# Kernel tuning notes

Hardware: AMD Instinct MI355X
Metric: run time of the kernel (lower is better)

Reference implementation:

```python
import jax, jax.numpy as jnp
import numpy as np

NUM_CLASSES = 5
SMOOTH = 1e-5


def setup_inputs() -> dict:
    key = jax.random.key(0)
    k1, k2, k3 = jax.random.split(key, 3)
    B, C, X, Y, Z = 2, NUM_CLASSES, 128, 128, 128
    net_output = jax.random.normal(k1, (B, C, X, Y, Z), dtype=jnp.float32)
    target = jax.random.randint(k2, (B, 1, X, Y, Z), 0, C, dtype=jnp.int64)
    dist = jax.random.uniform(k3, (B, 1, X, Y, Z), dtype=jnp.float32)
    return {"net_output": net_output, "target": target, "dist": dist}


def reference(net_output, target, dist):
    # --- Distance-map penalized multi-class Dice ---
    p = jax.nn.softmax(net_output, axis=1)  # (B,C,X,Y,Z)
    gt = target[:, 0]  # (B,X,Y,Z)
    classes = jnp.arange(NUM_CLASSES)[None, :, None, None, None]
    y_onehot = (gt[:, None] == classes).astype(p.dtype)  # (B,C,X,Y,Z)
    # per-class, per-batch sums over spatial dims
    tp = jnp.sum(p * y_onehot * dist, axis=(2, 3, 4))  # (B,C), dist broadcasts over C
    denom = jnp.sum(p, axis=(2, 3, 4)) + jnp.sum(y_onehot, axis=(2, 3, 4))  # (B,C)
    dc = (2.0 * tp + SMOOTH) / (denom + SMOOTH)  # (B,C)
    # sum over classes of batch-mean, divided by num_classes == overall mean
    dpdc_loss = -jnp.mean(dc)
    # --- Cross entropy (mean over all voxels), target squeezed to class idx ---
    logp = jax.nn.log_softmax(net_output, axis=1)  # (B,C,X,Y,Z)
    nll = -jnp.take_along_axis(logp, target, axis=1)  # (B,1,X,Y,Z)
    ce_loss = jnp.mean(nll)
    # aggregate == 'sum', weight_ce = weight_dice = 1
    return ce_loss + dpdc_loss
```

## Files before the change

kernel.cpp:

```cpp
#include <hip/hip_runtime.h>

#define NC 5
#define NB 2
#define SPATIAL (128*128*128)
#define TILE_VOX 512
#define NTILES (SPATIAL/TILE_VOX)
#define SMOOTHF 1e-5f

#define TILE_BYTES (16*1024)


__device__ __forceinline__ void async16(const char* g, char* l) {
    __builtin_amdgcn_global_load_lds(
        (const __attribute__((address_space(1))) void*)g,
        (__attribute__((address_space(3))) void*)l, 16, 0, 0);
}

__global__ __launch_bounds__(256) void dpdc_main(
    const float* __restrict__ net, const void* __restrict__ targ,
    const float* __restrict__ dist, float* __restrict__ slots, int TPB)
{
    __shared__ __align__(16) char lds[2][TILE_BYTES];
    const int b = blockIdx.y, tid = threadIdx.x;

    const unsigned long long tv = ((const unsigned long long*)targ)[tid & 63];
    const int t64 = (__ballot(tv >= 5ull) == 0ull);

    const char* netb  = (const char*)net  + (size_t)b * NC * SPATIAL * 4;
    const char* distb = (const char*)dist + (size_t)b * SPATIAL * 4;
    const char* targb = (const char*)targ + (size_t)b * SPATIAL * (t64 ? 8 : 4);

    const int tl0 = blockIdx.x * TPB;
    const int nchunk = t64 ? 1024 : 896;

    const char* srcp[4];
    int sstr[4];
    bool act[4];
    #pragma unroll
    for (int k = 0; k < 4; ++k) {
        const int q = tid + 256 * k;
        act[k] = (q < nchunk);
        const int r = q >> 7;
        if (r < 5) {
            srcp[k] = netb + (size_t)r * SPATIAL * 4
                           + (size_t)tl0 * 2048 + (size_t)(q & 127) * 16;
            sstr[k] = 2048;
        } else if (r == 5) {
            srcp[k] = distb + (size_t)tl0 * 2048 + (size_t)(q & 127) * 16;
            sstr[k] = 2048;
        } else {
            const int tstr = t64 ? 4096 : 2048;
            srcp[k] = targb + (size_t)tl0 * tstr + (size_t)(q - 768) * 16;
            sstr[k] = tstr;
        }
    }

    auto stage = [&](int bf) {
        char* base = &lds[bf][0];
        #pragma unroll
        for (int k = 0; k < 4; ++k)
            if (act[k]) async16(srcp[k], base + (size_t)(tid + 256 * k) * 16);
        #pragma unroll
        for (int k = 0; k < 4; ++k) srcp[k] += sstr[k];
    };

    float tp[NC], sp[NC], cnt[NC];
    #pragma unroll
    for (int c = 0; c < NC; ++c) { tp[c] = 0.f; sp[c] = 0.f; cnt[c] = 0.f; }
    float nll = 0.f;

    stage(0);
    __syncthreads();

    #pragma unroll 1
    for (int k = 0; k < TPB; ++k) {
        if (k + 1 < TPB) stage((k + 1) & 1);

        const char* base = &lds[k & 1][0];
        float2 l[NC];
        #pragma unroll
        for (int c = 0; c < NC; ++c)
            l[c] = *(const float2*)(base + c * 2048 + tid * 8);
        float2 dd = *(const float2*)(base + 10240 + tid * 8);
        int tt[2];
        if (t64) {
            ulonglong2 a = *(const ulonglong2*)(base + 12288 + tid * 16);
            tt[0] = (int)a.x; tt[1] = (int)a.y;
        } else {
            int2 a = *(const int2*)(base + 12288 + tid * 8);
            tt[0] = a.x; tt[1] = a.y;
        }
        const float* dv = (const float*)&dd;
        #pragma unroll
        for (int j = 0; j < 2; ++j) {
            float lc[NC];
            #pragma unroll
            for (int c = 0; c < NC; ++c) lc[c] = ((const float*)&l[c])[j];
            float m = fmaxf(fmaxf(fmaxf(lc[0], lc[1]), fmaxf(lc[2], lc[3])), lc[4]);
            float e[NC];
            float s = 0.f;
            #pragma unroll
            for (int c = 0; c < NC; ++c) { e[c] = __expf(lc[c] - m); s += e[c]; }
            float inv = 1.0f / s;
            int t = tt[j];
            float lsel = lc[4];
            #pragma unroll
            for (int c = 0; c < 4; ++c) lsel = (t == c) ? lc[c] : lsel;
            float pd = dv[j] * inv;
            #pragma unroll
            for (int c = 0; c < NC; ++c) {
                float p = e[c] * inv;
                sp[c] += p;
                tp[c] += (t == c) ? e[c] * pd : 0.f;
                cnt[c] += (t == c) ? 1.f : 0.f;
            }
            nll += __logf(s) - (lsel - m);
        }
        __syncthreads();
    }

    __shared__ float red[4][16];
    float vals[16];
    #pragma unroll
    for (int c = 0; c < NC; ++c) {
        vals[c] = tp[c]; vals[5 + c] = sp[c]; vals[10 + c] = cnt[c];
    }
    vals[15] = nll;
    const int lane = tid & 63;
    const int wave = tid >> 6;
    #pragma unroll
    for (int k = 0; k < 16; ++k) {
        float v = vals[k];
        #pragma unroll
        for (int off = 32; off > 0; off >>= 1) v += __shfl_down(v, off, 64);
        if (lane == 0) red[wave][k] = v;
    }
    __syncthreads();
    if (tid < 16) {
        float v = red[0][tid] + red[1][tid] + red[2][tid] + red[3][tid];
        slots[((size_t)b * gridDim.x + blockIdx.x) * 16 + tid] = v;
    }
}

__global__ __launch_bounds__(1024) void finalize(const float* __restrict__ slots,
                                                 int gx, float* __restrict__ out) {
    __shared__ float part[1024];
    __shared__ float tot[32];
    const int j = threadIdx.x;
    const int p = j & 31;
    const int b = p >> 4, k = p & 15;
    float s = 0.f;
    for (int slot = j >> 5; slot < gx; slot += 32)
        s += slots[((size_t)b * gx + slot) * 16 + k];
    part[j] = s;
    __syncthreads();
    if (j < 32) {
        float t = 0.f;
        #pragma unroll
        for (int m = 0; m < 32; ++m) t += part[j + 32 * m];
        tot[j] = t;
    }
    __syncthreads();
    if (j == 0) {
        float dcsum = 0.f;
        for (int bb = 0; bb < NB; ++bb)
            for (int c = 0; c < NC; ++c) {
                float tpv = tot[bb * 16 + c];
                float spv = tot[bb * 16 + 5 + c];
                float cv  = tot[bb * 16 + 10 + c];
                dcsum += (2.f * tpv + SMOOTHF) / (spv + cv + SMOOTHF);
            }
        float ce = (tot[15] + tot[31]) / (float)((size_t)NB * SPATIAL);
        out[0] = ce - dcsum / (float)(NB * NC);
    }
}

extern "C" void kernel_launch(void* const* d_in, const int* in_sizes, int n_in,
                              void* d_out, int out_size, void* d_ws, size_t ws_size,
                              hipStream_t stream) {
    const float* net  = (const float*)d_in[0];
    const void*  targ = d_in[1];
    const float* dist = (const float*)d_in[2];
    float* slots = (float*)d_ws;

    int gx = 512;
    while ((size_t)NB * gx * 16 * sizeof(float) > ws_size && gx > 1) gx >>= 1;
    const int tpb = NTILES / gx;

    dim3 grid(gx, NB);
    dpdc_main<<<grid, 256, 0, stream>>>(net, targ, dist, slots, tpb);
    finalize<<<1, 1024, 0, stream>>>(slots, gx, (float*)d_out);
}
```

Measured before the change: 34.80 us.

## Triple-buffer async LDS loads with explicit vmcnt waits instead of full syncs

```diff
diff --git a/kernel.cpp b/kernel.cpp
--- a/kernel.cpp
+++ b/kernel.cpp
@@ -6,6 +6,7 @@
 #define TILE_VOX 512
 #define NTILES (SPATIAL/TILE_VOX)
 #define SMOOTHF 1e-5f
+#define NBUF 3
 
 #define TILE_BYTES (16*1024)
 
@@ -16,11 +17,18 @@
         (__attribute__((address_space(3))) void*)l, 16, 0, 0);
 }
 
+__device__ __forceinline__ void wait_oldest(int stages) {
+    if (stages >= 3)      asm volatile("s_waitcnt vmcnt(8)" ::: "memory");
+    else if (stages == 2) asm volatile("s_waitcnt vmcnt(4)" ::: "memory");
+    else                  asm volatile("s_waitcnt vmcnt(0)" ::: "memory");
+    __builtin_amdgcn_sched_barrier(0);
+}
+
 __global__ __launch_bounds__(256) void dpdc_main(
     const float* __restrict__ net, const void* __restrict__ targ,
     const float* __restrict__ dist, float* __restrict__ slots, int TPB)
 {
-    __shared__ __align__(16) char lds[2][TILE_BYTES];
+    __shared__ __align__(16) char lds[NBUF][TILE_BYTES];
     const int b = blockIdx.y, tid = threadIdx.x;
 
     const unsigned long long tv = ((const unsigned long long*)targ)[tid & 63];
@@ -31,15 +39,13 @@
     const char* targb = (const char*)targ + (size_t)b * SPATIAL * (t64 ? 8 : 4);
 
     const int tl0 = blockIdx.x * TPB;
-    const int nchunk = t64 ? 1024 : 896;
+    const int tstr = t64 ? 4096 : 2048;
 
     const char* srcp[4];
     int sstr[4];
-    bool act[4];
     #pragma unroll
     for (int k = 0; k < 4; ++k) {
         const int q = tid + 256 * k;
-        act[k] = (q < nchunk);
         const int r = q >> 7;
         if (r < 5) {
             srcp[k] = netb + (size_t)r * SPATIAL * 4
@@ -49,8 +55,9 @@
             srcp[k] = distb + (size_t)tl0 * 2048 + (size_t)(q & 127) * 16;
             sstr[k] = 2048;
         } else {
-            const int tstr = t64 ? 4096 : 2048;
-            srcp[k] = targb + (size_t)tl0 * tstr + (size_t)(q - 768) * 16;
+            int tq = q - 768;
+            if (!t64 && tq >= 128) tq -= 128;
+            srcp[k] = targb + (size_t)tl0 * tstr + (size_t)tq * 16;
             sstr[k] = tstr;
         }
     }
@@ -58,10 +65,10 @@
     auto stage = [&](int bf) {
         char* base = &lds[bf][0];
         #pragma unroll
-        for (int k = 0; k < 4; ++k)
-            if (act[k]) async16(srcp[k], base + (size_t)(tid + 256 * k) * 16);
-        #pragma unroll
-        for (int k = 0; k < 4; ++k) srcp[k] += sstr[k];
+        for (int k = 0; k < 4; ++k) {
+            async16(srcp[k], base + (size_t)(tid + 256 * k) * 16);
+            srcp[k] += sstr[k];
+        }
     };
 
     float tp[NC], sp[NC], cnt[NC];
@@ -69,14 +76,17 @@
     for (int c = 0; c < NC; ++c) { tp[c] = 0.f; sp[c] = 0.f; cnt[c] = 0.f; }
     float nll = 0.f;
 
-    stage(0);
-    __syncthreads();
+    stage(0); stage(1); stage(2);
 
     #pragma unroll 1
     for (int k = 0; k < TPB; ++k) {
-        if (k + 1 < TPB) stage((k + 1) & 1);
-
-        const char* base = &lds[k & 1][0];
+        const int inflight = (TPB - k < 3) ? (TPB - k) : 3;
+        wait_oldest(inflight);
+        asm volatile("" ::: "memory");
+        __builtin_amdgcn_s_barrier();
+        asm volatile("" ::: "memory");
+
+        const char* base = &lds[k % NBUF][0];
         float2 l[NC];
         #pragma unroll
         for (int c = 0; c < NC; ++c)
@@ -116,7 +126,11 @@
             }
             nll += __logf(s) - (lsel - m);
         }
-        __syncthreads();
+
+        asm volatile("" ::: "memory");
+        __builtin_amdgcn_s_barrier();
+        asm volatile("" ::: "memory");
+        if (k + 3 < TPB) stage(k % NBUF);
     }
 
     __shared__ float red[4][16];
```

Result: slower. 38.44 us (+10.5%).
